# Optimization experiments

Hardware: AMD Instinct MI355X
Metric: run time of the kernel (lower is better)

Reference implementation:

```python
import jax, jax.numpy as jnp
import numpy as np
from jax import lax

# Dims (match init_kwargs)
NP, DP = 32, 8      # num_primary_a, dim_primary_a
NT, DT = 16, 16     # num_timecaps_a, dim_timecaps
KT = 3              # kernel_timecaps_a
EPS = 1e-7


def setup_inputs() -> dict:
    key = jax.random.key(0)
    k1, k2, k3 = jax.random.split(key, 3)
    B, T = 8, 1024
    x = jax.random.normal(k1, (B, T, NP, DP), dtype=jnp.float32)
    # Conv2D kernel: HWIO = [kernel_t, dim_primary_a, in_ch=1, out_ch=NT*DT]
    conv_kernel = jax.random.normal(k2, (KT, DP, 1, NT * DT), dtype=jnp.float32) * 0.05
    conv_bias = jnp.zeros((NT * DT,), dtype=jnp.float32)
    B_weight = jax.random.normal(k3, (T, NT, 1, NP), dtype=jnp.float32) * 0.05
    return {"x": x, "conv_kernel": conv_kernel, "conv_bias": conv_bias, "B_weight": B_weight}


def reference(x, conv_kernel, conv_bias, B_weight):
    B, T, Np, Dp = x.shape
    # reshape1: [B, T, Np*Dp, 1]
    xr = x.reshape(B, T, Np * Dp, 1)
    # Conv2D(filters=NT*DT, kernel=[KT, Dp], strides=[1, Dp], padding='same', relu)
    y = lax.conv_general_dilated(
        xr, conv_kernel,
        window_strides=(1, Dp), padding='SAME',
        dimension_numbers=('NHWC', 'HWIO', 'NHWC'))
    y = jax.nn.relu(y + conv_bias)  # [B, T, Np, NT*DT]
    # reshape2 + permute -> U_hat: [B, T, NT, Np, DT]
    U = y.reshape(B, T, Np, NT, DT).transpose(0, 1, 3, 2, 4)
    # self-similarity attention
    A = jnp.einsum('btnpd,btnqd->btnpq', U, U) / jnp.sqrt(jnp.float32(Dp))
    C = jax.nn.softmax(A.sum(axis=-2, keepdims=True), axis=-1)  # [B,T,NT,1,Np]
    out = jnp.einsum('btnop,btnpd->btnod', C + B_weight, U)  # [B,T,NT,1,DT]
    out = out[..., 0, :]  # squeeze axis=-2 -> [B,T,NT,DT]
    # squash
    norm = jnp.linalg.norm(out, axis=-1, keepdims=True)
    sq = norm * norm
    return (sq / (sq + 1.0)) * (out / (norm + EPS))
```

## Files before the change

### kernel.cpp

```cpp
#include <hip/hip_runtime.h>

#define T_DIM 1024

typedef short short8 __attribute__((ext_vector_type(8)));
typedef float f32x4  __attribute__((ext_vector_type(4)));

__device__ __forceinline__ unsigned pk_bf16(float lo, float hi) {
    unsigned r;
    asm("v_cvt_pk_bf16_f32 %0, %1, %2" : "=v"(r) : "v"(lo), "v"(hi));
    return r;
}

__global__ void kpack_kernel(const float* __restrict__ K, uint4* __restrict__ Kp) {
    const int col = threadIdx.x;
    #pragma unroll
    for (int kb = 0; kb < 4; ++kb) {
        uint4 wv = make_uint4(0u, 0u, 0u, 0u);
        if (kb < 3) {
            const float* kp = K + kb * 8 * 256 + col;
            wv.x = pk_bf16(kp[0 * 256], kp[1 * 256]);
            wv.y = pk_bf16(kp[2 * 256], kp[3 * 256]);
            wv.z = pk_bf16(kp[4 * 256], kp[5 * 256]);
            wv.w = pk_bf16(kp[6 * 256], kp[7 * 256]);
        }
        Kp[kb * 256 + col] = wv;
    }
}

__device__ __forceinline__ void wave_ds_fence() {
    __builtin_amdgcn_sched_barrier(0);
    asm volatile("s_waitcnt lgkmcnt(0)" ::: "memory");
    __builtin_amdgcn_sched_barrier(0);
}

__global__ __launch_bounds__(256, 4) void caps_kernel(
    const float* __restrict__ x,
    const float* __restrict__ bias,
    const float* __restrict__ Bw,
    const uint4* __restrict__ Kp,
    float* __restrict__ out)
{
    const int bt  = blockIdx.x;
    const int t   = bt & (T_DIM - 1);
    const int tid = threadIdx.x;
    const int l   = tid & 63;
    const int w   = tid >> 6;
    const int kb  = l >> 4;
    const int r16 = l & 15;

    __shared__ float Ut[256 * 36];
    __shared__ float Vs[256];
    __shared__ float cs[16 * 36];

    const int n = tid >> 4, j = tid & 15;
    const float bwj0 = Bw[(size_t)t * 512 + n * 32 + j];
    const float bwj1 = Bw[(size_t)t * 512 + n * 32 + 16 + j];

    const int  tt    = t + kb - 1;
    const bool valid = (kb < 3) && (tt >= 0) && (tt < T_DIM);
    short8 a[2];
    #pragma unroll
    for (int mi = 0; mi < 2; ++mi) {
        float4 x0 = make_float4(0.f, 0.f, 0.f, 0.f), x1 = x0;
        if (valid) {
            const float* xp = x + ((size_t)(bt + kb - 1) * 256 + (mi * 16 + r16) * 8);
            x0 = *reinterpret_cast<const float4*>(xp);
            x1 = *reinterpret_cast<const float4*>(xp + 4);
        }
        union { short8 s; uint4 u; } au;
        au.u.x = pk_bf16(x0.x, x0.y);
        au.u.y = pk_bf16(x0.z, x0.w);
        au.u.z = pk_bf16(x1.x, x1.y);
        au.u.w = pk_bf16(x1.z, x1.w);
        a[mi] = au.s;
    }

    short8 bfrag[4];
    float  bo[4];
    #pragma unroll
    for (int i = 0; i < 4; ++i) {
        const int col = w * 64 + i * 16 + r16;
        union { short8 s; uint4 u; } bu;
        bu.u = Kp[kb * 256 + col];
        bfrag[i] = bu.s;
        bo[i] = bias[col];
    }

    f32x4 acc[2][4];
    #pragma unroll
    for (int mi = 0; mi < 2; ++mi)
        #pragma unroll
        for (int i = 0; i < 4; ++i) {
            acc[mi][i] = (f32x4){0.f, 0.f, 0.f, 0.f};
            acc[mi][i] = __builtin_amdgcn_mfma_f32_16x16x32_bf16(
                a[mi], bfrag[i], acc[mi][i], 0, 0, 0);
        }

    const float is8 = 0.35355339059327373f;
    float vkeep = 0.f;
    #pragma unroll
    for (int i = 0; i < 4; ++i) {
        const int col = w * 64 + i * 16 + r16;
        float Uv[8];
        #pragma unroll
        for (int mi = 0; mi < 2; ++mi)
            #pragma unroll
            for (int e = 0; e < 4; ++e)
                Uv[mi * 4 + e] = fmaxf(acc[mi][i][e] + bo[i], 0.f);

        float vs = ((Uv[0] + Uv[1]) + (Uv[2] + Uv[3])) +
                   ((Uv[4] + Uv[5]) + (Uv[6] + Uv[7]));
        vs += __shfl_xor(vs, 16);
        vs += __shfl_xor(vs, 32);
        if (i == kb) vkeep = vs * is8;

        const int rot = 8 * (i & 3);
        #pragma unroll
        for (int mi = 0; mi < 2; ++mi) {
            const int slot = (mi * 16 + kb * 4 + rot) & 31;
            *reinterpret_cast<float4*>(&Ut[col * 36 + slot]) =
                make_float4(Uv[mi * 4], Uv[mi * 4 + 1], Uv[mi * 4 + 2], Uv[mi * 4 + 3]);
        }
    }
    Vs[tid] = vkeep;

    wave_ds_fence();

    const int rot2 = 8 * (n & 3);

    float4 u4[8];
    #pragma unroll
    for (int k = 0; k < 8; ++k)
        u4[k] = *reinterpret_cast<const float4*>(&Ut[tid * 36 + ((4 * k + rot2) & 31)]);

    const int slot0 = (j + rot2) & 31;
    const int slot1 = slot0 ^ 16;
    float s0 = 0.f, s1 = 0.f;
    #pragma unroll
    for (int kk = 0; kk < 4; ++kk) {
        const float4 vq = *reinterpret_cast<const float4*>(&Vs[n * 16 + 4 * kk]);
        const float* up = &Ut[(n * 16 + 4 * kk) * 36];
        s0 = fmaf(up[0 * 36 + slot0], vq.x, s0);  s1 = fmaf(up[0 * 36 + slot1], vq.x, s1);
        s0 = fmaf(up[1 * 36 + slot0], vq.y, s0);  s1 = fmaf(up[1 * 36 + slot1], vq.y, s1);
        s0 = fmaf(up[2 * 36 + slot0], vq.z, s0);  s1 = fmaf(up[2 * 36 + slot1], vq.z, s1);
        s0 = fmaf(up[3 * 36 + slot0], vq.w, s0);  s1 = fmaf(up[3 * 36 + slot1], vq.w, s1);
    }

    float m = fmaxf(s0, s1);
    #pragma unroll
    for (int mask = 1; mask <= 8; mask <<= 1) m = fmaxf(m, __shfl_xor(m, mask));
    const float e0 = __expf(s0 - m), e1 = __expf(s1 - m);
    float es = e0 + e1;
    #pragma unroll
    for (int mask = 1; mask <= 8; mask <<= 1) es += __shfl_xor(es, mask);
    const float inv = __builtin_amdgcn_rcpf(es);

    cs[n * 36 + slot0] = fmaf(e0, inv, bwj0);
    cs[n * 36 + slot1] = fmaf(e1, inv, bwj1);

    wave_ds_fence();

    float od = 0.f;
    #pragma unroll
    for (int k = 0; k < 8; ++k) {
        const float4 cq = *reinterpret_cast<const float4*>(&cs[n * 36 + ((4 * k + rot2) & 31)]);
        od = fmaf(cq.x, u4[k].x, od);
        od = fmaf(cq.y, u4[k].y, od);
        od = fmaf(cq.z, u4[k].z, od);
        od = fmaf(cq.w, u4[k].w, od);
    }

    float ss = od * od;
    #pragma unroll
    for (int mask = 1; mask <= 8; mask <<= 1) ss += __shfl_xor(ss, mask);
    const float nrm = sqrtf(ss);
    const float res = ss * __builtin_amdgcn_rcpf(ss + 1.f) *
                      (od * __builtin_amdgcn_rcpf(nrm + 1e-7f));

    out[(size_t)bt * 256 + tid] = res;
}

extern "C" void kernel_launch(void* const* d_in, const int* in_sizes, int n_in,
                              void* d_out, int out_size, void* d_ws, size_t ws_size,
                              hipStream_t stream) {
    const float* x    = (const float*)d_in[0];
    const float* K    = (const float*)d_in[1];
    const float* bias = (const float*)d_in[2];
    const float* Bw   = (const float*)d_in[3];
    float* out        = (float*)d_out;
    uint4* Kp         = (uint4*)d_ws;

    kpack_kernel<<<1, 256, 0, stream>>>(K, Kp);

    const int B  = in_sizes[0] / (T_DIM * 32 * 8);
    const int nb = B * T_DIM;
    caps_kernel<<<nb, 256, 0, stream>>>(x, bias, Bw, Kp, out);
}
```

Measured before the change: 40.28 us.

## Transpose MFMA operands, use XOR-swizzled row layout and DPP reductions

Swaps the MFMA operand roles so each lane holds four consecutive output dims of one primary capsule. It stores U row-major per capsule with an XOR swizzle to avoid LDS bank conflicts. Each thread loads its two capsule rows into registers and computes the V sums, logits, softmax and output with DPP row-rotate all-reductions over 16 lanes instead of ds_swizzle shuffles. This drops the Vs/cs shared buffers and the second LDS fence, at the cost of more redundant ALU work (16-wide reductions on every component) and a select chain to pick each lane's output.

After: 45.73 us. 13.5% more time.

```diff
diff --git a/kernel.cpp b/kernel.cpp
--- a/kernel.cpp
+++ b/kernel.cpp
@@ -27,10 +27,33 @@
     }
 }
 
+template <int N>
+__device__ __forceinline__ float rorN(float v) {
+    return __int_as_float(__builtin_amdgcn_update_dpp(
+        __float_as_int(v), __float_as_int(v), 0x120 | N, 0xF, 0xF, false));
+}
+__device__ __forceinline__ float allred_add16(float v) {
+    v += rorN<8>(v); v += rorN<4>(v); v += rorN<2>(v); v += rorN<1>(v);
+    return v;
+}
+__device__ __forceinline__ float allred_max16(float v) {
+    v = fmaxf(v, rorN<8>(v)); v = fmaxf(v, rorN<4>(v));
+    v = fmaxf(v, rorN<2>(v)); v = fmaxf(v, rorN<1>(v));
+    return v;
+}
+__device__ __forceinline__ void allred_add16_v4(f32x4& a) {
+    #pragma unroll
+    for (int c = 0; c < 4; ++c) a[c] = allred_add16(a[c]);
+}
+
 __device__ __forceinline__ void wave_ds_fence() {
     __builtin_amdgcn_sched_barrier(0);
     asm volatile("s_waitcnt lgkmcnt(0)" ::: "memory");
     __builtin_amdgcn_sched_barrier(0);
+}
+
+__device__ __forceinline__ int uidx(int q, int o) {
+    return q * 256 + ((((o) >> 2) ^ (q & 7)) << 2);
 }
 
 __global__ __launch_bounds__(256, 4) void caps_kernel(
@@ -48,134 +71,131 @@
     const int kb  = l >> 4;
     const int r16 = l & 15;
 
-    __shared__ float Ut[256 * 36];
-    __shared__ float Vs[256];
-    __shared__ float cs[16 * 36];
-
-    const int n = tid >> 4, j = tid & 15;
-    const float bwj0 = Bw[(size_t)t * 512 + n * 32 + j];
-    const float bwj1 = Bw[(size_t)t * 512 + n * 32 + 16 + j];
+    __shared__ float Urow[32 * 256];
 
     const int  tt    = t + kb - 1;
     const bool valid = (kb < 3) && (tt >= 0) && (tt < T_DIM);
-    short8 a[2];
-    #pragma unroll
-    for (int mi = 0; mi < 2; ++mi) {
+    short8 bx[2];
+    #pragma unroll
+    for (int qt = 0; qt < 2; ++qt) {
         float4 x0 = make_float4(0.f, 0.f, 0.f, 0.f), x1 = x0;
         if (valid) {
-            const float* xp = x + ((size_t)(bt + kb - 1) * 256 + (mi * 16 + r16) * 8);
+            const float* xp = x + ((size_t)(bt + kb - 1) * 256 + (qt * 16 + r16) * 8);
             x0 = *reinterpret_cast<const float4*>(xp);
             x1 = *reinterpret_cast<const float4*>(xp + 4);
         }
+        union { short8 s; uint4 u; } bu;
+        bu.u.x = pk_bf16(x0.x, x0.y);
+        bu.u.y = pk_bf16(x0.z, x0.w);
+        bu.u.z = pk_bf16(x1.x, x1.y);
+        bu.u.w = pk_bf16(x1.z, x1.w);
+        bx[qt] = bu.s;
+    }
+
+    short8 af[4];
+    f32x4  bo4[4];
+    #pragma unroll
+    for (int oti = 0; oti < 4; ++oti) {
         union { short8 s; uint4 u; } au;
-        au.u.x = pk_bf16(x0.x, x0.y);
-        au.u.y = pk_bf16(x0.z, x0.w);
-        au.u.z = pk_bf16(x1.x, x1.y);
-        au.u.w = pk_bf16(x1.z, x1.w);
-        a[mi] = au.s;
-    }
-
-    short8 bfrag[4];
-    float  bo[4];
-    #pragma unroll
-    for (int i = 0; i < 4; ++i) {
-        const int col = w * 64 + i * 16 + r16;
-        union { short8 s; uint4 u; } bu;
-        bu.u = Kp[kb * 256 + col];
-        bfrag[i] = bu.s;
-        bo[i] = bias[col];
+        au.u = Kp[kb * 256 + w * 64 + oti * 16 + r16];
+        af[oti] = au.s;
+        const float4 b4 = *reinterpret_cast<const float4*>(
+            &bias[w * 64 + oti * 16 + kb * 4]);
+        bo4[oti] = (f32x4){b4.x, b4.y, b4.z, b4.w};
     }
 
     f32x4 acc[2][4];
     #pragma unroll
-    for (int mi = 0; mi < 2; ++mi)
-        #pragma unroll
-        for (int i = 0; i < 4; ++i) {
-            acc[mi][i] = (f32x4){0.f, 0.f, 0.f, 0.f};
-            acc[mi][i] = __builtin_amdgcn_mfma_f32_16x16x32_bf16(
-                a[mi], bfrag[i], acc[mi][i], 0, 0, 0);
-        }
-
-    const float is8 = 0.35355339059327373f;
-    float vkeep = 0.f;
-    #pragma unroll
-    for (int i = 0; i < 4; ++i) {
-        const int col = w * 64 + i * 16 + r16;
-        float Uv[8];
-        #pragma unroll
-        for (int mi = 0; mi < 2; ++mi)
+    for (int qt = 0; qt < 2; ++qt)
+        #pragma unroll
+        for (int oti = 0; oti < 4; ++oti) {
+            acc[qt][oti] = (f32x4){0.f, 0.f, 0.f, 0.f};
+            acc[qt][oti] = __builtin_amdgcn_mfma_f32_16x16x32_bf16(
+                af[oti], bx[qt], acc[qt][oti], 0, 0, 0);
+        }
+
+    #pragma unroll
+    for (int qt = 0; qt < 2; ++qt) {
+        const int q = qt * 16 + r16;
+        #pragma unroll
+        for (int oti = 0; oti < 4; ++oti) {
+            const int obase = w * 64 + oti * 16 + kb * 4;
+            f32x4 uv;
             #pragma unroll
             for (int e = 0; e < 4; ++e)
-                Uv[mi * 4 + e] = fmaxf(acc[mi][i][e] + bo[i], 0.f);
-
-        float vs = ((Uv[0] + Uv[1]) + (Uv[2] + Uv[3])) +
-                   ((Uv[4] + Uv[5]) + (Uv[6] + Uv[7]));
-        vs += __shfl_xor(vs, 16);
-        vs += __shfl_xor(vs, 32);
-        if (i == kb) vkeep = vs * is8;
-
-        const int rot = 8 * (i & 3);
-        #pragma unroll
-        for (int mi = 0; mi < 2; ++mi) {
-            const int slot = (mi * 16 + kb * 4 + rot) & 31;
-            *reinterpret_cast<float4*>(&Ut[col * 36 + slot]) =
-                make_float4(Uv[mi * 4], Uv[mi * 4 + 1], Uv[mi * 4 + 2], Uv[mi * 4 + 3]);
-        }
-    }
-    Vs[tid] = vkeep;
+                uv[e] = fmaxf(acc[qt][oti][e] + bo4[oti][e], 0.f);
+            *reinterpret_cast<f32x4*>(&Urow[uidx(q, obase)]) = uv;
+        }
+    }
 
     wave_ds_fence();
 
-    const int rot2 = 8 * (n & 3);
-
-    float4 u4[8];
-    #pragma unroll
-    for (int k = 0; k < 8; ++k)
-        u4[k] = *reinterpret_cast<const float4*>(&Ut[tid * 36 + ((4 * k + rot2) & 31)]);
-
-    const int slot0 = (j + rot2) & 31;
-    const int slot1 = slot0 ^ 16;
+    const int n = tid >> 4, j = tid & 15;
+
+    f32x4 r0[4], r1[4];
+    #pragma unroll
+    for (int i = 0; i < 4; ++i) {
+        r0[i] = *reinterpret_cast<const f32x4*>(&Urow[uidx(j,      n * 16 + 4 * i)]);
+        r1[i] = *reinterpret_cast<const f32x4*>(&Urow[uidx(j + 16, n * 16 + 4 * i)]);
+    }
+
+    const float is8 = 0.35355339059327373f;
+    f32x4 V[4];
+    #pragma unroll
+    for (int i = 0; i < 4; ++i) {
+        V[i] = r0[i] + r1[i];
+        allred_add16_v4(V[i]);
+        #pragma unroll
+        for (int c = 0; c < 4; ++c) V[i][c] *= is8;
+    }
+
     float s0 = 0.f, s1 = 0.f;
     #pragma unroll
-    for (int kk = 0; kk < 4; ++kk) {
-        const float4 vq = *reinterpret_cast<const float4*>(&Vs[n * 16 + 4 * kk]);
-        const float* up = &Ut[(n * 16 + 4 * kk) * 36];
-        s0 = fmaf(up[0 * 36 + slot0], vq.x, s0);  s1 = fmaf(up[0 * 36 + slot1], vq.x, s1);
-        s0 = fmaf(up[1 * 36 + slot0], vq.y, s0);  s1 = fmaf(up[1 * 36 + slot1], vq.y, s1);
-        s0 = fmaf(up[2 * 36 + slot0], vq.z, s0);  s1 = fmaf(up[2 * 36 + slot1], vq.z, s1);
-        s0 = fmaf(up[3 * 36 + slot0], vq.w, s0);  s1 = fmaf(up[3 * 36 + slot1], vq.w, s1);
-    }
-
-    float m = fmaxf(s0, s1);
-    #pragma unroll
-    for (int mask = 1; mask <= 8; mask <<= 1) m = fmaxf(m, __shfl_xor(m, mask));
+    for (int i = 0; i < 4; ++i)
+        #pragma unroll
+        for (int c = 0; c < 4; ++c) {
+            s0 = fmaf(V[i][c], r0[i][c], s0);
+            s1 = fmaf(V[i][c], r1[i][c], s1);
+        }
+
+    const float m  = allred_max16(fmaxf(s0, s1));
     const float e0 = __expf(s0 - m), e1 = __expf(s1 - m);
-    float es = e0 + e1;
-    #pragma unroll
-    for (int mask = 1; mask <= 8; mask <<= 1) es += __shfl_xor(es, mask);
+    const float es = allred_add16(e0 + e1);
     const float inv = __builtin_amdgcn_rcpf(es);
 
-    cs[n * 36 + slot0] = fmaf(e0, inv, bwj0);
-    cs[n * 36 + slot1] = fmaf(e1, inv, bwj1);
-
-    wave_ds_fence();
-
-    float od = 0.f;
-    #pragma unroll
-    for (int k = 0; k < 8; ++k) {
-        const float4 cq = *reinterpret_cast<const float4*>(&cs[n * 36 + ((4 * k + rot2) & 31)]);
-        od = fmaf(cq.x, u4[k].x, od);
-        od = fmaf(cq.y, u4[k].y, od);
-        od = fmaf(cq.z, u4[k].z, od);
-        od = fmaf(cq.w, u4[k].w, od);
-    }
-
-    float ss = od * od;
-    #pragma unroll
-    for (int mask = 1; mask <= 8; mask <<= 1) ss += __shfl_xor(ss, mask);
+    const float* bwp = Bw + (size_t)t * 512 + n * 32;
+    const float c0 = fmaf(e0, inv, bwp[j]);
+    const float c1 = fmaf(e1, inv, bwp[j + 16]);
+
+    f32x4 op[4];
+    #pragma unroll
+    for (int i = 0; i < 4; ++i) {
+        #pragma unroll
+        for (int c = 0; c < 4; ++c)
+            op[i][c] = fmaf(c0, r0[i][c], c1 * r1[i][c]);
+        allred_add16_v4(op[i]);
+    }
+
+    float ss = 0.f;
+    #pragma unroll
+    for (int i = 0; i < 4; ++i)
+        #pragma unroll
+        for (int c = 0; c < 4; ++c) ss = fmaf(op[i][c], op[i][c], ss);
+
+    float csel[4];
+    #pragma unroll
+    for (int i = 0; i < 4; ++i) {
+        const float lo = (j & 1) ? op[i][1] : op[i][0];
+        const float hi = (j & 1) ? op[i][3] : op[i][2];
+        csel[i] = (j & 2) ? hi : lo;
+    }
+    const float oxa = (j & 4) ? csel[1] : csel[0];
+    const float oxb = (j & 4) ? csel[3] : csel[2];
+    const float ox  = (j & 8) ? oxb : oxa;
+
     const float nrm = sqrtf(ss);
     const float res = ss * __builtin_amdgcn_rcpf(ss + 1.f) *
-                      (od * __builtin_amdgcn_rcpf(nrm + 1e-7f));
+                      (ox * __builtin_amdgcn_rcpf(nrm + 1e-7f));
 
     out[(size_t)bt * 256 + tid] = res;
 }
```
